# Kernel tuning notes

Hardware: AMD Instinct MI355X
Metric: run time of the kernel (lower is better)

The kernel has to match this reference:

```python
import jax, jax.numpy as jnp
import numpy as np

NUM_CLASSES = 50000
NUM_SAMPLED = 1000
D_MODEL = 1024
BATCH, SEQ = 32, 512


def _log_expected_count(ids, num_sampled, num_classes):
    # TF log-uniform candidate sampler (unique=True):
    # P(c) = log((c+2)/(c+1)) / log(num_classes+1)
    # E[count] = -expm1(num_sampled * log1p(-P))
    ids_f = ids.astype(jnp.float32)
    p = (jnp.log(ids_f + 2.0) - jnp.log(ids_f + 1.0)) / np.float32(np.log(num_classes + 1.0))
    return jnp.log(-jnp.expm1(num_sampled * jnp.log1p(-p)))


def setup_inputs() -> dict:
    key = jax.random.key(0)
    k1, k2, k3, k4 = jax.random.split(key, 4)
    lstm_outputs = jax.random.normal(k1, (BATCH, SEQ, D_MODEL), dtype=jnp.float32)
    next_token_ids = jax.random.randint(k2, (BATCH, SEQ), 0, NUM_CLASSES)
    sampled_ids = jax.random.randint(k3, (BATCH, NUM_SAMPLED), 0, NUM_CLASSES)
    W = jax.random.normal(k4, (NUM_CLASSES, D_MODEL), dtype=jnp.float32) * (1.0 / np.sqrt(D_MODEL))
    b = jnp.zeros((NUM_CLASSES,), dtype=jnp.float32)
    return {"lstm_outputs": lstm_outputs, "next_token_ids": next_token_ids,
            "sampled_ids": sampled_ids, "W": W, "b": b}


def reference(lstm_outputs, next_token_ids, sampled_ids, W, b):
    # Vectorized sampled-softmax loss (tf.nn.sampled_softmax_loss with
    # log-uniform sampler, partition_strategy irrelevant, accidental-hit removal),
    # mapped over the batch dim as the original tf.map_fn does.
    log_q_true = _log_expected_count(next_token_ids, NUM_SAMPLED, NUM_CLASSES)   # [B,T]
    log_q_samp = _log_expected_count(sampled_ids, NUM_SAMPLED, NUM_CLASSES)      # [B,S]

    w_true = W[next_token_ids]                                                   # [B,T,D]
    true_logit = (jnp.einsum('btd,btd->bt', lstm_outputs, w_true)
                  + b[next_token_ids] - log_q_true)                              # [B,T]

    w_samp = W[sampled_ids]                                                      # [B,S,D]
    samp_logits = (jnp.einsum('btd,bsd->bts', lstm_outputs, w_samp)
                   + b[sampled_ids][:, None, :] - log_q_samp[:, None, :])        # [B,T,S]

    # remove accidental hits (sampled id == true label)
    hit = sampled_ids[:, None, :] == next_token_ids[:, :, None]                  # [B,T,S]
    samp_logits = jnp.where(hit, jnp.float32(-1e9), samp_logits)

    all_logits = jnp.concatenate([true_logit[..., None], samp_logits], axis=-1)  # [B,T,1+S]
    # softmax CE with true class at index 0
    losses = jax.nn.logsumexp(all_logits, axis=-1) - true_logit                  # [B,T]
    return 0.5 * jnp.mean(losses)
```

## Files before the change

kernel.cpp:

```cpp
#include <hip/hip_runtime.h>
#include <cmath>

#define BATCH 32
#define SEQLEN 512
#define NSAMP 1000
#define DMODEL 1024
#define NCHUNK 4

typedef __bf16 bf16x8_t __attribute__((ext_vector_type(8)));
typedef float f32x4_t __attribute__((ext_vector_type(4)));

__device__ __forceinline__ unsigned pack_bf2(float lo, float hi) {
    unsigned ulo = __float_as_uint(lo);
    unsigned uhi = __float_as_uint(hi);
    ulo = (ulo + 0x7fffu + ((ulo >> 16) & 1u)) >> 16;
    uhi = (uhi + 0x7fffu + ((uhi >> 16) & 1u)) & 0xffff0000u;
    return (ulo & 0xffffu) | uhi;
}

__device__ __forceinline__ float log_expected_count(int id) {
    float idf = (float)id;
    float p = log1pf(1.0f / (idf + 1.0f)) * 0.09242316f;
    return logf(-expm1f(1000.0f * log1pf(-p)));
}

__device__ __forceinline__ void gl16(const void* g, void* l) {
    __builtin_amdgcn_global_load_lds(
        (const __attribute__((address_space(1))) unsigned int*)g,
        (__attribute__((address_space(3))) unsigned int*)l,
        16, 0, 0);
}

__global__ __launch_bounds__(256) void prep_kernel(
    const float* __restrict__ h, const int* __restrict__ labels,
    const float* __restrict__ W, const float* __restrict__ bias,
    unsigned short* __restrict__ hb, float* __restrict__ tlw)
{
    const int w = threadIdx.x >> 6, lane = threadIdx.x & 63;
    const int r = blockIdx.x * 4 + w;
    const int lab = labels[r];
    const float4* hp = (const float4*)(h + (size_t)r * DMODEL);
    const float4* wp = (const float4*)(W + (size_t)lab * DMODEL);
    unsigned short* hdst = hb + (size_t)r * DMODEL;
    float s = 0.0f;
#pragma unroll
    for (int j = 0; j < 4; ++j) {
        float4 a = hp[lane + j * 64];
        float4 c = wp[lane + j * 64];
        s += a.x * c.x + a.y * c.y + a.z * c.z + a.w * c.w;
        uint2 u;
        u.x = pack_bf2(a.x, a.y);
        u.y = pack_bf2(a.z, a.w);
        *(uint2*)(hdst + (lane + j * 64) * 4) = u;
    }
#pragma unroll
    for (int off = 32; off > 0; off >>= 1) s += __shfl_xor(s, off, 64);
    if (lane == 0) tlw[r] = s + bias[lab] - log_expected_count(lab);
}

__global__ __launch_bounds__(512, 2) void sampled_softmax_main(
    const int* __restrict__ labels, const int* __restrict__ sids,
    const unsigned short* __restrict__ hb, const float* __restrict__ W,
    const float* __restrict__ bias,
    float* __restrict__ pm, float* __restrict__ pl)
{
    __shared__ __align__(16) unsigned short Ab[2][256 * 64];
    __shared__ __align__(16) unsigned short Bb[2][256 * 64];
    __shared__ int   sid_lds[256];
    __shared__ float adj_lds[256];
    __shared__ int   lab_lds[256];
    __shared__ float mpart[4][256];
    __shared__ float lpart[4][256];

    const int wg     = blockIdx.x;
    const int bb     = wg & 31;
    const int rest   = wg >> 5;
    const int tile_t = rest & 1;
    const int chunk  = rest >> 1;
    const int t0  = tile_t * 256;
    const int tid = threadIdx.x;
    const int wv  = tid >> 6, l = tid & 63;
    const int wr  = wv >> 2, wc = wv & 3;
    const int lm  = l & 15,  q = l >> 4;
    const int rl8 = l >> 3,  cp8 = l & 7;

    if (tid < 256) {
        const int s = chunk * 256 + tid;
        if (s < NSAMP) {
            const int sv = sids[bb * NSAMP + s];
            sid_lds[tid] = sv;
            adj_lds[tid] = bias[sv] - log_expected_count(sv);
        } else {
            sid_lds[tid] = -1;
            adj_lds[tid] = 0.0f;
        }
        lab_lds[tid] = labels[bb * SEQLEN + t0 + tid];
    }

    const int csg = (cp8 ^ rl8) * 8;
    const unsigned short* aSrc = hb + (size_t)(bb * SEQLEN + t0 + 32 * wv + rl8) * DMODEL + csg;

    const float* wsrc[4];
    int bwoff[4];
#pragma unroll
    for (int j = 0; j < 4; ++j) {
        int rb = chunk * 256 + 32 * wv + 8 * j + rl8;
        if (rb > NSAMP - 1) rb = NSAMP - 1;
        const int sv = sids[bb * NSAMP + rb];
        wsrc[j] = W + (size_t)sv * DMODEL + cp8 * 8;
        bwoff[j] = (32 * wv + 8 * j + rl8) * 64 + (cp8 ^ rl8) * 8;
    }

    float4 br[8];
#define LOAD_B(KT)                                                            \
    do {                                                                      \
        br[0] = *(const float4*)(wsrc[0] + (KT) * 64);                        \
        br[1] = *(const float4*)(wsrc[0] + (KT) * 64 + 4);                    \
        br[2] = *(const float4*)(wsrc[1] + (KT) * 64);                        \
        br[3] = *(const float4*)(wsrc[1] + (KT) * 64 + 4);                    \
        br[4] = *(const float4*)(wsrc[2] + (KT) * 64);                        \
        br[5] = *(const float4*)(wsrc[2] + (KT) * 64 + 4);                    \
        br[6] = *(const float4*)(wsrc[3] + (KT) * 64);                        \
        br[7] = *(const float4*)(wsrc[3] + (KT) * 64 + 4);                    \
    } while (0)

#define PACK_WRITE_B(BUF)                                                     \
    do {                                                                      \
        _Pragma("unroll")                                                     \
        for (int j = 0; j < 4; ++j) {                                         \
            uint4 u;                                                          \
            u.x = pack_bf2(br[2 * j].x, br[2 * j].y);                         \
            u.y = pack_bf2(br[2 * j].z, br[2 * j].w);                         \
            u.z = pack_bf2(br[2 * j + 1].x, br[2 * j + 1].y);                 \
            u.w = pack_bf2(br[2 * j + 1].z, br[2 * j + 1].w);                 \
            *(uint4*)&Bb[BUF][bwoff[j]] = u;                                  \
        }                                                                     \
    } while (0)

#define STAGE_A(KT, BUF)                                                      \
    do {                                                                      \
        const size_t _adv = (size_t)(KT) * 64;                                \
        gl16(aSrc + _adv,               &Ab[BUF][(32 * wv     ) * 64]);       \
        gl16(aSrc + 8 * DMODEL + _adv,  &Ab[BUF][(32 * wv +  8) * 64]);       \
        gl16(aSrc + 16 * DMODEL + _adv, &Ab[BUF][(32 * wv + 16) * 64]);       \
        gl16(aSrc + 24 * DMODEL + _adv, &Ab[BUF][(32 * wv + 24) * 64]);       \
    } while (0)

    const int ck0 = ((0 + q) ^ (lm & 7)) * 8;
    const int ck1 = ((4 + q) ^ (lm & 7)) * 8;
    int rowA[8], rowB[4];
#pragma unroll
    for (int t = 0; t < 8; ++t) rowA[t] = (128 * wr + 16 * t + lm) * 64;
#pragma unroll
    for (int c = 0; c < 4; ++c) rowB[c] = (64 * wc + 16 * c + lm) * 64;

    f32x4_t acc[8][4];
#pragma unroll
    for (int t = 0; t < 8; ++t)
#pragma unroll
        for (int c = 0; c < 4; ++c) acc[t][c] = (f32x4_t){0.f, 0.f, 0.f, 0.f};

    LOAD_B(0);
    __builtin_amdgcn_sched_barrier(0);
    STAGE_A(0, 0);
    asm volatile("s_waitcnt vmcnt(0)" ::: "memory");
    PACK_WRITE_B(0);
    asm volatile("s_waitcnt lgkmcnt(0)" ::: "memory");
    __builtin_amdgcn_s_barrier();

#pragma unroll
    for (int kt = 0; kt < 16; ++kt) {
        const int cur = kt & 1, nxt = cur ^ 1;
        if (kt + 1 < 16) {
            LOAD_B(kt + 1);
            __builtin_amdgcn_sched_barrier(0);
            STAGE_A(kt + 1, nxt);
            asm volatile("s_waitcnt vmcnt(12)" ::: "memory");
        } else {
            asm volatile("s_waitcnt vmcnt(0)" ::: "memory");
        }

        const unsigned short* Ac = Ab[cur];
        const unsigned short* Bc = Bb[cur];
#pragma unroll
        for (int s = 0; s < 2; ++s) {
            const int ck = s ? ck1 : ck0;
            bf16x8_t fa[8];
#pragma unroll
            for (int t = 0; t < 8; ++t) fa[t] = *(const bf16x8_t*)(Ac + rowA[t] + ck);
            __builtin_amdgcn_s_setprio(1);
#pragma unroll
            for (int c = 0; c < 4; ++c) {
                bf16x8_t fb = *(const bf16x8_t*)(Bc + rowB[c] + ck);
#pragma unroll
                for (int t = 0; t < 8; ++t)
                    acc[t][c] = __builtin_amdgcn_mfma_f32_16x16x32_bf16(fa[t], fb, acc[t][c], 0, 0, 0);
            }
            __builtin_amdgcn_s_setprio(0);
        }

        if (kt + 1 < 16) {
            asm volatile("s_waitcnt vmcnt(4)" ::: "memory");
            PACK_WRITE_B(nxt);
            asm volatile("s_waitcnt lgkmcnt(0)" ::: "memory");
            __builtin_amdgcn_s_barrier();
        }
    }
#undef LOAD_B
#undef PACK_WRITE_B
#undef STAGE_A

    float adjv[4]; int sidv[4]; bool cval[4];
#pragma unroll
    for (int c = 0; c < 4; ++c) {
        const int col = 64 * wc + 16 * c + lm;
        adjv[c] = adj_lds[col];
        sidv[c] = sid_lds[col];
        cval[c] = (chunk * 256 + col) < NSAMP;
    }
#pragma unroll
    for (int t = 0; t < 8; ++t) {
#pragma unroll
        for (int i = 0; i < 4; ++i) {
            const int r = 128 * wr + 16 * t + 4 * q + i;
            const int lab = lab_lds[r];
            float x[4]; bool ok[4];
            float m = -INFINITY;
#pragma unroll
            for (int c = 0; c < 4; ++c) {
                x[c] = acc[t][c][i] + adjv[c];
                ok[c] = cval[c] && (sidv[c] != lab);
                if (ok[c]) m = fmaxf(m, x[c]);
            }
            float ls = 0.0f;
#pragma unroll
            for (int c = 0; c < 4; ++c) ls += ok[c] ? __expf(x[c] - m) : 0.0f;
#pragma unroll
            for (int off = 1; off < 16; off <<= 1) {
                const float mo = __shfl_xor(m, off, 64);
                const float lo = __shfl_xor(ls, off, 64);
                const float M  = fmaxf(m, mo);
                const float e1 = (ls > 0.0f) ? ls * __expf(m - M) : 0.0f;
                const float e2 = (lo > 0.0f) ? lo * __expf(mo - M) : 0.0f;
                m = M; ls = e1 + e2;
            }
            if (lm == 0) { mpart[wc][r] = m; lpart[wc][r] = ls; }
        }
    }
    __syncthreads();
    if (tid < 256) {
        float m = -INFINITY, lsum = 0.0f;
#pragma unroll
        for (int p = 0; p < 4; ++p) {
            const float mp = mpart[p][tid];
            const float lp = lpart[p][tid];
            if (lp > 0.0f) {
                if (mp > m) { lsum = lsum * __expf(m - mp) + lp; m = mp; }
                else        { lsum += lp * __expf(mp - m); }
            }
        }
        const int idx = (bb * SEQLEN + t0 + tid) * NCHUNK + chunk;
        pm[idx] = m;
        pl[idx] = lsum;
    }
}

__global__ __launch_bounds__(256) void combine_kernel(
    const float* __restrict__ pm, const float* __restrict__ pl,
    const float* __restrict__ tlw, float* __restrict__ bsum)
{
    __shared__ float wsum[4];
    const int tid = threadIdx.x;
    const int w = tid >> 6, lane = tid & 63;
    const int idx = blockIdx.x * 256 + tid;
    float m = -INFINITY, l = 0.0f;
#pragma unroll
    for (int c = 0; c < NCHUNK; ++c) {
        const float mp = pm[idx * NCHUNK + c];
        const float lp = pl[idx * NCHUNK + c];
        if (lp > 0.0f) {
            if (mp > m) { l = l * __expf(m - mp) + lp; m = mp; }
            else        { l += lp * __expf(mp - m); }
        }
    }
    const float t = tlw[idx];
    const float M = fmaxf(m, t);
    float loss = __logf(l * __expf(m - M) + __expf(t - M)) + M - t;
#pragma unroll
    for (int off = 32; off > 0; off >>= 1) loss += __shfl_xor(loss, off, 64);
    if (lane == 0) wsum[w] = loss;
    __syncthreads();
    if (tid == 0) bsum[blockIdx.x] = wsum[0] + wsum[1] + wsum[2] + wsum[3];
}

__global__ void finalize_kernel(const float* __restrict__ bsum, float* __restrict__ out) {
    float v = bsum[threadIdx.x];
#pragma unroll
    for (int off = 32; off > 0; off >>= 1) v += __shfl_xor(v, off, 64);
    if (threadIdx.x == 0) out[0] = v * (0.5f / (float)(BATCH * SEQLEN));
}

extern "C" void kernel_launch(void* const* d_in, const int* in_sizes, int n_in,
                              void* d_out, int out_size, void* d_ws, size_t ws_size,
                              hipStream_t stream) {
    const float* h      = (const float*)d_in[0];
    const int*   labels = (const int*)d_in[1];
    const int*   sids   = (const int*)d_in[2];
    const float* W      = (const float*)d_in[3];
    const float* bias   = (const float*)d_in[4];

    char* base = (char*)d_ws;
    unsigned short* hb = (unsigned short*)base;
    float* tlw  = (float*)(base + 33554432);
    float* pmw  = (float*)(base + 33619968);
    float* plw  = (float*)(base + 33882112);
    float* bsum = (float*)(base + 34144256);

    prep_kernel<<<dim3(4096), dim3(256), 0, stream>>>(h, labels, W, bias, hb, tlw);
    sampled_softmax_main<<<dim3(256), dim3(512), 0, stream>>>(
        labels, sids, hb, W, bias, pmw, plw);
    combine_kernel<<<dim3(64), dim3(256), 0, stream>>>(pmw, plw, tlw, bsum);
    finalize_kernel<<<dim3(1), dim3(64), 0, stream>>>(bsum, (float*)d_out);
}
```

Before: 375.2 us.

## Retile main GEMM to 512x128 tiles with K-step 32 and eight sample chunks

Each workgroup now covers the full 512-token sequence for one batch against a 128-sample chunk, where before it covered a 256x256 tile. Eight chunks replace four, so the grid stays at 256 workgroups. The K step shrinks from 64 to 32, which halves LDS per stage and uses a new XOR swizzle, but doubles the number of loop iterations and barriers. The intent is to gather each W row fewer times per token and to cut per-thread staging registers, at the cost of more hidden-state reloads across chunks and more synchronization. Partial-result buffers and workspace offsets grow to hold the extra chunks.

```diff
diff --git a/kernel.cpp b/kernel.cpp
--- a/kernel.cpp
+++ b/kernel.cpp
@@ -5,7 +5,7 @@
 #define SEQLEN 512
 #define NSAMP 1000
 #define DMODEL 1024
-#define NCHUNK 4
+#define NCHUNK 8
 
 typedef __bf16 bf16x8_t __attribute__((ext_vector_type(8)));
 typedef float f32x4_t __attribute__((ext_vector_type(4)));
@@ -64,95 +64,82 @@
     const float* __restrict__ bias,
     float* __restrict__ pm, float* __restrict__ pl)
 {
-    __shared__ __align__(16) unsigned short Ab[2][256 * 64];
-    __shared__ __align__(16) unsigned short Bb[2][256 * 64];
-    __shared__ int   sid_lds[256];
-    __shared__ float adj_lds[256];
-    __shared__ int   lab_lds[256];
-    __shared__ float mpart[4][256];
-    __shared__ float lpart[4][256];
-
-    const int wg     = blockIdx.x;
-    const int bb     = wg & 31;
-    const int rest   = wg >> 5;
-    const int tile_t = rest & 1;
-    const int chunk  = rest >> 1;
-    const int t0  = tile_t * 256;
+    __shared__ __align__(16) unsigned short Ab[2][512 * 32];
+    __shared__ __align__(16) unsigned short Bb[2][128 * 32];
+    __shared__ int   sid_lds[128];
+    __shared__ float adj_lds[128];
+    __shared__ int   lab_lds[512];
+    __shared__ float mpart[2][512];
+    __shared__ float lpart[2][512];
+
+    const int wg    = blockIdx.x;
+    const int bb    = wg & 31;
+    const int chunk = wg >> 5;
     const int tid = threadIdx.x;
     const int wv  = tid >> 6, l = tid & 63;
-    const int wr  = wv >> 2, wc = wv & 3;
+    const int wr  = wv >> 1, wc = wv & 1;
     const int lm  = l & 15,  q = l >> 4;
-    const int rl8 = l >> 3,  cp8 = l & 7;
-
-    if (tid < 256) {
-        const int s = chunk * 256 + tid;
-        if (s < NSAMP) {
-            const int sv = sids[bb * NSAMP + s];
-            sid_lds[tid] = sv;
-            adj_lds[tid] = bias[sv] - log_expected_count(sv);
-        } else {
-            sid_lds[tid] = -1;
-            adj_lds[tid] = 0.0f;
-        }
-        lab_lds[tid] = labels[bb * SEQLEN + t0 + tid];
-    }
-
-    const int csg = (cp8 ^ rl8) * 8;
-    const unsigned short* aSrc = hb + (size_t)(bb * SEQLEN + t0 + 32 * wv + rl8) * DMODEL + csg;
-
-    const float* wsrc[4];
-    int bwoff[4];
-#pragma unroll
-    for (int j = 0; j < 4; ++j) {
-        int rb = chunk * 256 + 32 * wv + 8 * j + rl8;
-        if (rb > NSAMP - 1) rb = NSAMP - 1;
-        const int sv = sids[bb * NSAMP + rb];
-        wsrc[j] = W + (size_t)sv * DMODEL + cp8 * 8;
-        bwoff[j] = (32 * wv + 8 * j + rl8) * 64 + (cp8 ^ rl8) * 8;
-    }
-
-    float4 br[8];
+    const int rl4 = l >> 2,  cp = l & 3;
+
+    {
+        if (tid < 128) {
+            const int s = chunk * 128 + tid;
+            if (s < NSAMP) {
+                const int sv = sids[bb * NSAMP + s];
+                sid_lds[tid] = sv;
+                adj_lds[tid] = bias[sv] - log_expected_count(sv);
+            } else {
+                sid_lds[tid] = -1;
+                adj_lds[tid] = 0.0f;
+            }
+        }
+        lab_lds[tid] = labels[bb * SEQLEN + tid];
+    }
+
+    const int swzs = (rl4 & 3) ^ ((rl4 >> 2) & 3);
+    const int csA = (cp ^ swzs) * 8;
+    const unsigned short* aSrc = hb + (size_t)(bb * SEQLEN + 64 * wv + rl4) * DMODEL + csA;
+
+    const int brow = tid >> 2, bkc = tid & 3;
+    int rbg = chunk * 128 + brow;
+    if (rbg > NSAMP - 1) rbg = NSAMP - 1;
+    const float* wsrc = W + (size_t)sids[bb * NSAMP + rbg] * DMODEL + bkc * 8;
+    const int sB = (brow & 3) ^ ((brow >> 2) & 3);
+    const int bwoff = brow * 32 + (bkc ^ sB) * 8;
+
+    float4 br0, br1;
 #define LOAD_B(KT)                                                            \
     do {                                                                      \
-        br[0] = *(const float4*)(wsrc[0] + (KT) * 64);                        \
-        br[1] = *(const float4*)(wsrc[0] + (KT) * 64 + 4);                    \
-        br[2] = *(const float4*)(wsrc[1] + (KT) * 64);                        \
-        br[3] = *(const float4*)(wsrc[1] + (KT) * 64 + 4);                    \
-        br[4] = *(const float4*)(wsrc[2] + (KT) * 64);                        \
-        br[5] = *(const float4*)(wsrc[2] + (KT) * 64 + 4);                    \
-        br[6] = *(const float4*)(wsrc[3] + (KT) * 64);                        \
-        br[7] = *(const float4*)(wsrc[3] + (KT) * 64 + 4);                    \
+        br0 = *(const float4*)(wsrc + (KT) * 32);                             \
+        br1 = *(const float4*)(wsrc + (KT) * 32 + 4);                         \
     } while (0)
 
 #define PACK_WRITE_B(BUF)                                                     \
     do {                                                                      \
-        _Pragma("unroll")                                                     \
-        for (int j = 0; j < 4; ++j) {                                         \
-            uint4 u;                                                          \
-            u.x = pack_bf2(br[2 * j].x, br[2 * j].y);                         \
-            u.y = pack_bf2(br[2 * j].z, br[2 * j].w);                         \
-            u.z = pack_bf2(br[2 * j + 1].x, br[2 * j + 1].y);                 \
-            u.w = pack_bf2(br[2 * j + 1].z, br[2 * j + 1].w);                 \
-            *(uint4*)&Bb[BUF][bwoff[j]] = u;                                  \
-        }                                                                     \
+        uint4 u;                                                              \
+        u.x = pack_bf2(br0.x, br0.y);                                         \
+        u.y = pack_bf2(br0.z, br0.w);                                         \
+        u.z = pack_bf2(br1.x, br1.y);                                         \
+        u.w = pack_bf2(br1.z, br1.w);                                         \
+        *(uint4*)&Bb[BUF][bwoff] = u;                                         \
     } while (0)
 
 #define STAGE_A(KT, BUF)                                                      \
     do {                                                                      \
-        const size_t _adv = (size_t)(KT) * 64;                                \
-        gl16(aSrc + _adv,               &Ab[BUF][(32 * wv     ) * 64]);       \
-        gl16(aSrc + 8 * DMODEL + _adv,  &Ab[BUF][(32 * wv +  8) * 64]);       \
-        gl16(aSrc + 16 * DMODEL + _adv, &Ab[BUF][(32 * wv + 16) * 64]);       \
-        gl16(aSrc + 24 * DMODEL + _adv, &Ab[BUF][(32 * wv + 24) * 64]);       \
+        const size_t _adv = (size_t)(KT) * 32;                                \
+        gl16(aSrc + _adv,                &Ab[BUF][(64 * wv     ) * 32]);      \
+        gl16(aSrc + 16 * DMODEL + _adv,  &Ab[BUF][(64 * wv + 16) * 32]);      \
+        gl16(aSrc + 32 * DMODEL + _adv,  &Ab[BUF][(64 * wv + 32) * 32]);      \
+        gl16(aSrc + 48 * DMODEL + _adv,  &Ab[BUF][(64 * wv + 48) * 32]);      \
     } while (0)
 
-    const int ck0 = ((0 + q) ^ (lm & 7)) * 8;
-    const int ck1 = ((4 + q) ^ (lm & 7)) * 8;
-    int rowA[8], rowB[4];
-#pragma unroll
-    for (int t = 0; t < 8; ++t) rowA[t] = (128 * wr + 16 * t + lm) * 64;
-#pragma unroll
-    for (int c = 0; c < 4; ++c) rowB[c] = (64 * wc + 16 * c + lm) * 64;
+    const int fswz = (lm & 3) ^ ((lm >> 2) & 3);
+    const int ck = (q ^ fswz) * 8;
+    int aoff[8], boff[4];
+#pragma unroll
+    for (int t = 0; t < 8; ++t) aoff[t] = (128 * wr + 16 * t + lm) * 32 + ck;
+#pragma unroll
+    for (int c = 0; c < 4; ++c) boff[c] = (64 * wc + 16 * c + lm) * 32 + ck;
 
     f32x4_t acc[8][4];
 #pragma unroll
@@ -169,37 +156,33 @@
     __builtin_amdgcn_s_barrier();
 
 #pragma unroll
-    for (int kt = 0; kt < 16; ++kt) {
+    for (int kt = 0; kt < 32; ++kt) {
         const int cur = kt & 1, nxt = cur ^ 1;
-        if (kt + 1 < 16) {
+        if (kt + 1 < 32) {
             LOAD_B(kt + 1);
             __builtin_amdgcn_sched_barrier(0);
             STAGE_A(kt + 1, nxt);
-            asm volatile("s_waitcnt vmcnt(12)" ::: "memory");
+            asm volatile("s_waitcnt vmcnt(6)" ::: "memory");
         } else {
             asm volatile("s_waitcnt vmcnt(0)" ::: "memory");
         }
 
         const unsigned short* Ac = Ab[cur];
         const unsigned short* Bc = Bb[cur];
-#pragma unroll
-        for (int s = 0; s < 2; ++s) {
-            const int ck = s ? ck1 : ck0;
-            bf16x8_t fa[8];
-#pragma unroll
-            for (int t = 0; t < 8; ++t) fa[t] = *(const bf16x8_t*)(Ac + rowA[t] + ck);
-            __builtin_amdgcn_s_setprio(1);
-#pragma unroll
-            for (int c = 0; c < 4; ++c) {
-                bf16x8_t fb = *(const bf16x8_t*)(Bc + rowB[c] + ck);
-#pragma unroll
-                for (int t = 0; t < 8; ++t)
-                    acc[t][c] = __builtin_amdgcn_mfma_f32_16x16x32_bf16(fa[t], fb, acc[t][c], 0, 0, 0);
-            }
-            __builtin_amdgcn_s_setprio(0);
-        }
-
-        if (kt + 1 < 16) {
+        bf16x8_t fa[8];
+#pragma unroll
+        for (int t = 0; t < 8; ++t) fa[t] = *(const bf16x8_t*)(Ac + aoff[t]);
+        __builtin_amdgcn_s_setprio(1);
+#pragma unroll
+        for (int c = 0; c < 4; ++c) {
+            bf16x8_t fb = *(const bf16x8_t*)(Bc + boff[c]);
+#pragma unroll
+            for (int t = 0; t < 8; ++t)
+                acc[t][c] = __builtin_amdgcn_mfma_f32_16x16x32_bf16(fa[t], fb, acc[t][c], 0, 0, 0);
+        }
+        __builtin_amdgcn_s_setprio(0);
+
+        if (kt + 1 < 32) {
             asm volatile("s_waitcnt vmcnt(4)" ::: "memory");
             PACK_WRITE_B(nxt);
             asm volatile("s_waitcnt lgkmcnt(0)" ::: "memory");
@@ -216,7 +199,7 @@
         const int col = 64 * wc + 16 * c + lm;
         adjv[c] = adj_lds[col];
         sidv[c] = sid_lds[col];
-        cval[c] = (chunk * 256 + col) < NSAMP;
+        cval[c] = (chunk * 128 + col) < NSAMP;
     }
 #pragma unroll
     for (int t = 0; t < 8; ++t) {
@@ -248,10 +231,10 @@
         }
     }
     __syncthreads();
-    if (tid < 256) {
+    {
         float m = -INFINITY, lsum = 0.0f;
 #pragma unroll
-        for (int p = 0; p < 4; ++p) {
+        for (int p = 0; p < 2; ++p) {
             const float mp = mpart[p][tid];
             const float lp = lpart[p][tid];
             if (lp > 0.0f) {
@@ -259,7 +242,7 @@
                 else        { lsum += lp * __expf(mp - m); }
             }
         }
-        const int idx = (bb * SEQLEN + t0 + tid) * NCHUNK + chunk;
+        const int idx = (bb * SEQLEN + tid) * NCHUNK + chunk;
         pm[idx] = m;
         pl[idx] = lsum;
     }
@@ -313,8 +296,8 @@
     unsigned short* hb = (unsigned short*)base;
     float* tlw  = (float*)(base + 33554432);
     float* pmw  = (float*)(base + 33619968);
-    float* plw  = (float*)(base + 33882112);
-    float* bsum = (float*)(base + 34144256);
+    float* plw  = (float*)(base + 34144256);
+    float* bsum = (float*)(base + 34668544);
 
     prep_kernel<<<dim3(4096), dim3(256), 0, stream>>>(h, labels, W, bias, hb, tlw);
     sampled_softmax_main<<<dim3(256), dim3(512), 0, stream>>>(
```

Result: no change. 379.7 us (+1.2%).
